# Kernel tuning notes

Hardware: AMD Instinct MI355X
Metric: run time of the kernel (lower is better)

## Reference

```python
import jax, jax.numpy as jnp
import numpy as np

N_NODES = 10000
N_EDGES = 200000
NODE_DIM = 128
EDGE_DIM = 16
CONV_DIM = 64
HEADS = 5
NEG_SLOPE = 0.2


def gatv2_layer(x, src, dst, edge_attr, Wl, bl, We, att, bias):
    # PyG GATv2Conv, share_weights=True, concat=False, add_self_loops=True, eval mode
    N = x.shape[0]
    H, C = att.shape
    xl = (x @ Wl + bl).reshape(N, H, C)  # [N,H,C]; x_r = x_l (share_weights)
    # self loops, edge_attr fill_value='mean' (mean of incoming edge_attr per node)
    deg = jax.ops.segment_sum(jnp.ones(dst.shape[0], x.dtype), dst, num_segments=N)
    loop_attr = jax.ops.segment_sum(edge_attr, dst, num_segments=N) / jnp.maximum(deg, 1.0)[:, None]
    loop = jnp.arange(N, dtype=src.dtype)
    src_f = jnp.concatenate([src, loop])
    dst_f = jnp.concatenate([dst, loop])
    ea = jnp.concatenate([edge_attr, loop_attr], axis=0)
    e_emb = (ea @ We).reshape(-1, H, C)  # [E+N,H,C]
    m = jax.nn.leaky_relu(xl[src_f] + xl[dst_f] + e_emb, NEG_SLOPE)
    score = jnp.einsum('ehc,hc->eh', m, att)  # [E+N,H]
    # per-destination softmax over incoming edges
    smax = jax.ops.segment_max(score, dst_f, num_segments=N)
    ex = jnp.exp(score - smax[dst_f])
    denom = jax.ops.segment_sum(ex, dst_f, num_segments=N)
    alpha = ex / denom[dst_f]
    out = jax.ops.segment_sum(alpha[:, :, None] * xl[src_f], dst_f, num_segments=N)
    return out.mean(axis=1) + bias  # concat=False -> mean over heads


def setup_inputs() -> dict:
    key = jax.random.key(0)
    ks = jax.random.split(key, 32)
    inp = {
        'x': jax.random.normal(ks[0], (N_NODES, NODE_DIM), jnp.float32),
        'edge_index': jax.random.randint(ks[1], (2, N_EDGES), 0, N_NODES, dtype=jnp.int32),
        'edge_attr': jax.random.normal(ks[2], (N_EDGES, EDGE_DIM), jnp.float32),
    }
    in_dims = [NODE_DIM, CONV_DIM, CONV_DIM]
    HC = HEADS * CONV_DIM
    k = 3
    for l in range(3):
        d = in_dims[l]
        inp[f'Wl{l}'] = jax.random.normal(ks[k], (d, HC), jnp.float32) / np.float32(np.sqrt(d)); k += 1
        inp[f'bl{l}'] = jnp.zeros((HC,), jnp.float32)
        inp[f'We{l}'] = jax.random.normal(ks[k], (EDGE_DIM, HC), jnp.float32) / np.float32(np.sqrt(EDGE_DIM)); k += 1
        inp[f'att{l}'] = jax.random.normal(ks[k], (HEADS, CONV_DIM), jnp.float32) / np.float32(np.sqrt(CONV_DIM)); k += 1
        inp[f'b{l}'] = jnp.zeros((CONV_DIM,), jnp.float32)
    return inp


def reference(x, edge_index, edge_attr,
              Wl0, bl0, We0, att0, b0,
              Wl1, bl1, We1, att1, b1,
              Wl2, bl2, We2, att2, b2):
    src, dst = edge_index[0], edge_index[1]
    h = x
    layers = [(Wl0, bl0, We0, att0, b0), (Wl1, bl1, We1, att1, b1), (Wl2, bl2, We2, att2, b2)]
    for Wl, bl, We, att, b in layers:
        h = gatv2_layer(h, src, dst, edge_attr, Wl, bl, We, att, b)
        h = jax.nn.elu(h)
    return h
```

## Files before the change

### kernel.cpp

```cpp
#include <hip/hip_runtime.h>
#include <hip/hip_bf16.h>


#define NN 10000
#define NE 200000
#define ND 128
#define ED 16
#define CD 64
#define NH 5
#define HC 320
#define EF 210000
#define EFP 210048
#define NEG 0.2f
#define PB 824
#define TOTB 4120
#define PERX 515

typedef float f2 __attribute__((ext_vector_type(2)));

__global__ void k_count(const int* __restrict__ dst, int* __restrict__ deg) {
  int e = blockIdx.x * blockDim.x + threadIdx.x;
  if (e >= NE) return;
  atomicAdd(&deg[dst[e]], 1);
}

__global__ __launch_bounds__(1024) void k_scan(const int* __restrict__ deg,
                                               int* __restrict__ rowptr) {
  __shared__ int part[1024];
  int t = threadIdx.x;
  int base = t * 10;
  int local[10];
  int s = 0;
  #pragma unroll
  for (int j = 0; j < 10; j++) {
    int i = base + j;
    local[j] = (i < NN) ? deg[i] : 0;
    s += local[j];
  }
  part[t] = s;
  __syncthreads();
  for (int off = 1; off < 1024; off <<= 1) {
    int v = (t >= off) ? part[t - off] : 0;
    __syncthreads();
    part[t] += v;
    __syncthreads();
  }
  int prefix = (t > 0) ? part[t - 1] : 0;
  #pragma unroll
  for (int j = 0; j < 10; j++) {
    int i = base + j;
    if (i < NN) rowptr[i] = prefix;
    prefix += local[j];
  }
  if (t == 1023) rowptr[NN] = prefix;
}

__global__ void k_fill(const int* __restrict__ ei, const int* __restrict__ rowptr,
                       int* __restrict__ cursor, int* __restrict__ csr_eid,
                       int* __restrict__ csr_src, int* __restrict__ csr_dst) {
  int e = blockIdx.x * blockDim.x + threadIdx.x;
  if (e >= NE) return;
  int d = ei[NE + e];
  int slot = atomicAdd(&cursor[d], 1);
  int pos = rowptr[d] + slot;
  csr_eid[pos] = e;
  csr_src[pos] = ei[e];
  csr_dst[pos] = d;
}

__global__ __launch_bounds__(256) void k_loopattr(const int* __restrict__ csr_eid,
                                                  const int* __restrict__ rowptr,
                                                  const float* __restrict__ eattr,
                                                  float* __restrict__ loop_attr) {
  int wave = threadIdx.x >> 6, lane = threadIdx.x & 63;
  int d = blockIdx.x * 4 + wave;
  if (d >= NN) return;
  int g = lane >> 4, k = lane & 15;
  int b = rowptr[d], n = rowptr[d + 1] - b;
  float s = 0.f;
  for (int i = g; i < n; i += 4)
    s += eattr[(size_t)csr_eid[b + i] * ED + k];
  s += __shfl_xor(s, 16, 64);
  s += __shfl_xor(s, 32, 64);
  if (g == 0) loop_attr[d * ED + k] = s / fmaxf((float)n, 1.0f);
}

__global__ void k_eacsr(const int* __restrict__ csr_eid, const float* __restrict__ eattr,
                        float* __restrict__ ea_csr) {
  int idx = blockIdx.x * blockDim.x + threadIdx.x;
  if (idx >= NE * 4) return;
  int p = idx >> 2, q = idx & 3;
  const float4* sp = (const float4*)(eattr + (size_t)csr_eid[p] * ED);
  ((float4*)(ea_csr + (size_t)p * ED))[q] = sp[q];
}

__global__ void k_wet(const float* __restrict__ We, float* __restrict__ Wpk) {
  int i = blockIdx.x * blockDim.x + threadIdx.x;
  if (i >= ED * HC) return;
  int j  = i & 1;
  int k  = (i >> 1) & 15;
  int cp = (i >> 5) & 31;
  int h  = i >> 10;
  Wpk[i] = We[k * HC + h * CD + cp * 2 + j];
}

template <int D>
__global__ __launch_bounds__(320) void k_xl(const float* __restrict__ h,
                                            const float* __restrict__ Wl,
                                            const float* __restrict__ bl,
                                            float* __restrict__ xl) {
  constexpr int NPB = 8;
  int node0 = blockIdx.x * NPB;
  int t = threadIdx.x;
  float acc[NPB];
  #pragma unroll
  for (int i = 0; i < NPB; i++) acc[i] = 0.f;
  for (int k = 0; k < D; k += 4) {
    float w0 = Wl[(k + 0) * HC + t];
    float w1 = Wl[(k + 1) * HC + t];
    float w2 = Wl[(k + 2) * HC + t];
    float w3 = Wl[(k + 3) * HC + t];
    #pragma unroll
    for (int i = 0; i < NPB; i++) {
      float4 hv = *(const float4*)(h + (size_t)(node0 + i) * D + k);
      acc[i] += hv.x * w0 + hv.y * w1 + hv.z * w2 + hv.w * w3;
    }
  }
  float bv = bl[t];
  int hh = t >> 6, c = t & 63;
  #pragma unroll
  for (int i = 0; i < NPB; i++)
    xl[((size_t)hh * NN + node0 + i) * CD + c] = acc[i] + bv;
}

__global__ __launch_bounds__(256) void k_score(
    const int* __restrict__ csr_src, const int* __restrict__ csr_dst,
    const float* __restrict__ ea_csr, const float* __restrict__ loop_attr,
    const float* __restrict__ xl, const float* __restrict__ Wpk,
    const float* __restrict__ att, float* __restrict__ wP) {
  int bid = blockIdx.x;
  int w = (bid & 7) * PERX + (bid >> 3);
  int h = w / PB;
  int lb = w - h * PB;
  int p = lb * 256 + threadIdx.x;
  if (p >= EF) return;
  int s, d;
  const float* ea;
  if (p < NE) { s = csr_src[p]; d = csr_dst[p]; ea = ea_csr + (size_t)p * ED; }
  else        { s = d = p - NE; ea = loop_attr + (size_t)(p - NE) * ED; }
  float eas[16];
  {
    const float4* q = (const float4*)ea;
    float4 t0 = q[0], t1 = q[1], t2 = q[2], t3 = q[3];
    eas[0] = t0.x;  eas[1] = t0.y;  eas[2] = t0.z;  eas[3] = t0.w;
    eas[4] = t1.x;  eas[5] = t1.y;  eas[6] = t1.z;  eas[7] = t1.w;
    eas[8] = t2.x;  eas[9] = t2.y;  eas[10] = t2.z; eas[11] = t2.w;
    eas[12] = t3.x; eas[13] = t3.y; eas[14] = t3.z; eas[15] = t3.w;
  }
  const float* xsrow = xl + ((size_t)h * NN + s) * CD;
  const float* xdrow = xl + ((size_t)h * NN + d) * CD;
  const f2* wp = (const f2*)Wpk + (size_t)h * (CD / 2) * ED;
  const f2* ap = (const f2*)(att + (size_t)h * CD);
  f2 sc2 = {0.f, 0.f};
  const f2 zero = {0.f, 0.f};
  #pragma unroll 4
  for (int cb = 0; cb < CD; cb += 4) {
    int cp = cb >> 1;
    float4 xs4 = *(const float4*)(xsrow + cb);
    float4 xd4 = *(const float4*)(xdrow + cb);
    const f2* w0 = wp + (size_t)cp * ED;
    const f2* w1 = w0 + ED;
    f2 z0 = f2{xs4.x, xs4.y} + f2{xd4.x, xd4.y};
    f2 z1 = f2{xs4.z, xs4.w} + f2{xd4.z, xd4.w};
    #pragma unroll
    for (int k = 0; k < ED; k++) {
      z0 += w0[k] * eas[k];
      z1 += w1[k] * eas[k];
    }
    z0 = __builtin_elementwise_max(z0, zero) + NEG * __builtin_elementwise_min(z0, zero);
    z1 = __builtin_elementwise_max(z1, zero) + NEG * __builtin_elementwise_min(z1, zero);
    sc2 += z0 * ap[cp];
    sc2 += z1 * ap[cp + 1];
  }
  float sc = sc2.x + sc2.y;
  sc = fminf(fmaxf(sc, -60.f), 60.f);
  wP[(size_t)h * EFP + p] = __expf(sc);
}

__global__ __launch_bounds__(320) void k_agg(
    const int* __restrict__ csr_src, const int* __restrict__ rowptr,
    const float* __restrict__ wP, const float* __restrict__ xl,
    const float* __restrict__ bias, float* __restrict__ out) {
  __shared__ float s_v[NH][CD];
  int h = threadIdx.x >> 6, lane = threadIdx.x & 63;
  int d = blockIdx.x;
  int b = rowptr[d], n = rowptr[d + 1] - b;
  const float* sp = wP + (size_t)h * EFP;
  const float* xlh = xl + (size_t)h * NN * CD + lane;
  float dn = sp[NE + d];
  float acc = dn * xlh[(size_t)d * CD];
  int p = b, pe = b + n;
  for (; p + 4 <= pe; p += 4) {
    int s0 = csr_src[p], s1 = csr_src[p + 1], s2 = csr_src[p + 2], s3 = csr_src[p + 3];
    float w0 = sp[p], w1 = sp[p + 1], w2 = sp[p + 2], w3 = sp[p + 3];
    float x0 = xlh[(size_t)s0 * CD];
    float x1 = xlh[(size_t)s1 * CD];
    float x2 = xlh[(size_t)s2 * CD];
    float x3 = xlh[(size_t)s3 * CD];
    dn += (w0 + w1) + (w2 + w3);
    acc += w0 * x0 + w1 * x1 + w2 * x2 + w3 * x3;
  }
  for (; p < pe; p++) {
    int s0 = csr_src[p];
    float w0 = sp[p];
    dn += w0;
    acc += w0 * xlh[(size_t)s0 * CD];
  }
  s_v[h][lane] = acc / dn;
  __syncthreads();
  if (h == 0) {
    float v = s_v[0][lane] + s_v[1][lane] + s_v[2][lane] + s_v[3][lane] + s_v[4][lane];
    v = v * (1.0f / NH) + bias[lane];
    v = v > 0.f ? v : expm1f(v);
    out[(size_t)d * CD + lane] = v;
  }
}

extern "C" void kernel_launch(void* const* d_in, const int* in_sizes, int n_in,
                              void* d_out, int out_size, void* d_ws, size_t ws_size,
                              hipStream_t stream) {
  const float* x = (const float*)d_in[0];
  const int* ei = (const int*)d_in[1];
  const float* eattr = (const float*)d_in[2];

  char* w = (char*)d_ws;
  int* degi      = (int*)w;                 w += NN * 4;
  int* cursor    = (int*)w;                 w += NN * 4;
  int* rowptr    = (int*)w;                 w += (NN + 1) * 4;
  int* csr_eid   = (int*)w;                 w += NE * 4;
  int* csr_src   = (int*)w;                 w += NE * 4;
  int* csr_dst   = (int*)w;                 w += NE * 4;
  float* loop_attr = (float*)w;             w += (size_t)NN * ED * 4;
  float* ea_csr  = (float*)w;               w += (size_t)NE * ED * 4;
  float* xl      = (float*)w;               w += (size_t)NN * HC * 4;
  float* wPbuf   = (float*)w;               w += (size_t)NH * EFP * 4;
  float* Wpk     = (float*)w;               w += (size_t)ED * HC * 4;
  float* hbuf    = (float*)w;               w += (size_t)NN * CD * 4;

  hipMemsetAsync(degi, 0, NN * 4, stream);
  hipMemsetAsync(cursor, 0, NN * 4, stream);
  k_count<<<(NE + 255) / 256, 256, 0, stream>>>(ei + NE, degi);
  k_scan<<<1, 1024, 0, stream>>>(degi, rowptr);
  k_fill<<<(NE + 255) / 256, 256, 0, stream>>>(ei, rowptr, cursor, csr_eid, csr_src, csr_dst);
  k_loopattr<<<(NN + 3) / 4, 256, 0, stream>>>(csr_eid, rowptr, eattr, loop_attr);
  k_eacsr<<<(NE * 4 + 255) / 256, 256, 0, stream>>>(csr_eid, eattr, ea_csr);

  for (int l = 0; l < 3; l++) {
    const float* Wl  = (const float*)d_in[3 + 5 * l];
    const float* bl  = (const float*)d_in[4 + 5 * l];
    const float* We  = (const float*)d_in[5 + 5 * l];
    const float* att = (const float*)d_in[6 + 5 * l];
    const float* b   = (const float*)d_in[7 + 5 * l];

    k_wet<<<(ED * HC + 255) / 256, 256, 0, stream>>>(We, Wpk);
    if (l == 0) k_xl<ND><<<NN / 8, 320, 0, stream>>>(x, Wl, bl, xl);
    else        k_xl<CD><<<NN / 8, 320, 0, stream>>>(hbuf, Wl, bl, xl);

    k_score<<<TOTB, 256, 0, stream>>>(csr_src, csr_dst, ea_csr, loop_attr,
                                      xl, Wpk, att, wPbuf);

    float* dst_out = (l < 2) ? hbuf : (float*)d_out;
    k_agg<<<NN, 320, 0, stream>>>(csr_src, rowptr, wPbuf, xl, b, dst_out);
  }
}
```

Before: 520.3 us.

## Restructure edge scoring to map channels to lanes with LDS reduction

The score kernel now assigns one channel per lane and 32 edges per wave instead of one edge per thread looping over all 64 channels. Each lane keeps its We column in registers, so the packed-weight kernel is removed. Edge attributes are interleaved in pairs and self-loop entries are folded into extended src/dst/ea arrays. Per-edge dot products are reduced through LDS, which makes xl row gathers coalesced across lanes. In exchange it adds a transpose through LDS, a shuffle, and extra preprocessing kernels.

```diff
diff --git a/kernel.cpp b/kernel.cpp
--- a/kernel.cpp
+++ b/kernel.cpp
@@ -12,9 +12,9 @@
 #define EF 210000
 #define EFP 210048
 #define NEG 0.2f
-#define PB 824
-#define TOTB 4120
-#define PERX 515
+#define WPH 1641
+#define TOT2 8205
+#define G2 8208
 
 typedef float f2 __attribute__((ext_vector_type(2)));
 
@@ -57,15 +57,24 @@
 
 __global__ void k_fill(const int* __restrict__ ei, const int* __restrict__ rowptr,
                        int* __restrict__ cursor, int* __restrict__ csr_eid,
-                       int* __restrict__ csr_src, int* __restrict__ csr_dst) {
+                       int* __restrict__ srcx, int* __restrict__ dstx) {
   int e = blockIdx.x * blockDim.x + threadIdx.x;
   if (e >= NE) return;
   int d = ei[NE + e];
   int slot = atomicAdd(&cursor[d], 1);
   int pos = rowptr[d] + slot;
   csr_eid[pos] = e;
-  csr_src[pos] = ei[e];
-  csr_dst[pos] = d;
+  srcx[pos] = ei[e];
+  dstx[pos] = d;
+}
+
+__global__ void k_selfext(int* __restrict__ srcx, int* __restrict__ dstx) {
+  int i = blockIdx.x * blockDim.x + threadIdx.x;
+  int p = NE + i;
+  if (p >= EFP) return;
+  int v = (p < EF) ? (p - NE) : 0;
+  srcx[p] = v;
+  dstx[p] = v;
 }
 
 __global__ __launch_bounds__(256) void k_loopattr(const int* __restrict__ csr_eid,
@@ -85,23 +94,16 @@
   if (g == 0) loop_attr[d * ED + k] = s / fmaxf((float)n, 1.0f);
 }
 
-__global__ void k_eacsr(const int* __restrict__ csr_eid, const float* __restrict__ eattr,
-                        float* __restrict__ ea_csr) {
+__global__ void k_ea2(const int* __restrict__ csr_eid, const float* __restrict__ eattr,
+                      const float* __restrict__ loop_attr, float* __restrict__ ea2) {
   int idx = blockIdx.x * blockDim.x + threadIdx.x;
-  if (idx >= NE * 4) return;
-  int p = idx >> 2, q = idx & 3;
-  const float4* sp = (const float4*)(eattr + (size_t)csr_eid[p] * ED);
-  ((float4*)(ea_csr + (size_t)p * ED))[q] = sp[q];
-}
-
-__global__ void k_wet(const float* __restrict__ We, float* __restrict__ Wpk) {
-  int i = blockIdx.x * blockDim.x + threadIdx.x;
-  if (i >= ED * HC) return;
-  int j  = i & 1;
-  int k  = (i >> 1) & 15;
-  int cp = (i >> 5) & 31;
-  int h  = i >> 10;
-  Wpk[i] = We[k * HC + h * CD + cp * 2 + j];
+  if (idx >= EFP * ED) return;
+  int p = idx >> 4, k = idx & 15;
+  float v;
+  if (p < NE)      v = eattr[(size_t)csr_eid[p] * ED + k];
+  else if (p < EF) v = loop_attr[(size_t)(p - NE) * ED + k];
+  else             v = 0.f;
+  ea2[((size_t)(p >> 1) * 32) + 2 * k + (p & 1)] = v;
 }
 
 template <int D>
@@ -134,57 +136,63 @@
 }
 
 __global__ __launch_bounds__(256) void k_score(
-    const int* __restrict__ csr_src, const int* __restrict__ csr_dst,
-    const float* __restrict__ ea_csr, const float* __restrict__ loop_attr,
-    const float* __restrict__ xl, const float* __restrict__ Wpk,
-    const float* __restrict__ att, float* __restrict__ wP) {
-  int bid = blockIdx.x;
-  int w = (bid & 7) * PERX + (bid >> 3);
-  int h = w / PB;
-  int lb = w - h * PB;
-  int p = lb * 256 + threadIdx.x;
-  if (p >= EF) return;
-  int s, d;
-  const float* ea;
-  if (p < NE) { s = csr_src[p]; d = csr_dst[p]; ea = ea_csr + (size_t)p * ED; }
-  else        { s = d = p - NE; ea = loop_attr + (size_t)(p - NE) * ED; }
-  float eas[16];
-  {
-    const float4* q = (const float4*)ea;
-    float4 t0 = q[0], t1 = q[1], t2 = q[2], t3 = q[3];
-    eas[0] = t0.x;  eas[1] = t0.y;  eas[2] = t0.z;  eas[3] = t0.w;
-    eas[4] = t1.x;  eas[5] = t1.y;  eas[6] = t1.z;  eas[7] = t1.w;
-    eas[8] = t2.x;  eas[9] = t2.y;  eas[10] = t2.z; eas[11] = t2.w;
-    eas[12] = t3.x; eas[13] = t3.y; eas[14] = t3.z; eas[15] = t3.w;
-  }
-  const float* xsrow = xl + ((size_t)h * NN + s) * CD;
-  const float* xdrow = xl + ((size_t)h * NN + d) * CD;
-  const f2* wp = (const f2*)Wpk + (size_t)h * (CD / 2) * ED;
-  const f2* ap = (const f2*)(att + (size_t)h * CD);
-  f2 sc2 = {0.f, 0.f};
+    const int* __restrict__ srcx, const int* __restrict__ dstx,
+    const float* __restrict__ ea2, const float* __restrict__ xl,
+    const float* __restrict__ We, const float* __restrict__ att,
+    float* __restrict__ wP) {
+  __shared__ float lds[4][64][34];
+  int wk = (blockIdx.x & 7) * 1026 + (blockIdx.x >> 3);
+  if (wk >= TOT2) return;
+  int h  = wk / WPH;
+  int lb = wk - h * WPH;
+  int wave = __builtin_amdgcn_readfirstlane(threadIdx.x >> 6);
+  int lane = threadIdx.x & 63;
+  int p0 = lb * 128 + wave * 32;
+
+  f2 wv[16];
+  #pragma unroll
+  for (int k = 0; k < 16; k++) {
+    float w = We[k * HC + h * CD + lane];
+    wv[k] = f2{w, w};
+  }
+  float a1 = att[h * CD + lane];
+  f2 av = f2{a1, a1};
+  const float* xh = xl + (size_t)h * NN * CD;
   const f2 zero = {0.f, 0.f};
-  #pragma unroll 4
-  for (int cb = 0; cb < CD; cb += 4) {
-    int cp = cb >> 1;
-    float4 xs4 = *(const float4*)(xsrow + cb);
-    float4 xd4 = *(const float4*)(xdrow + cb);
-    const f2* w0 = wp + (size_t)cp * ED;
-    const f2* w1 = w0 + ED;
-    f2 z0 = f2{xs4.x, xs4.y} + f2{xd4.x, xd4.y};
-    f2 z1 = f2{xs4.z, xs4.w} + f2{xd4.z, xd4.w};
+
+  f2 acc[16];
+  #pragma unroll
+  for (int i = 0; i < 16; i++) {
+    int p = p0 + 2 * i;
+    int s0 = srcx[p], s1 = srcx[p + 1];
+    int d0 = dstx[p], d1 = dstx[p + 1];
+    const f2* e = (const f2*)(ea2 + (size_t)(p >> 1) * 32);
+    float xs0 = xh[(size_t)s0 * CD + lane];
+    float xs1 = xh[(size_t)s1 * CD + lane];
+    float xd0 = xh[(size_t)d0 * CD + lane];
+    float xd1 = xh[(size_t)d1 * CD + lane];
+    f2 z = f2{xs0 + xd0, xs1 + xd1};
     #pragma unroll
-    for (int k = 0; k < ED; k++) {
-      z0 += w0[k] * eas[k];
-      z1 += w1[k] * eas[k];
-    }
-    z0 = __builtin_elementwise_max(z0, zero) + NEG * __builtin_elementwise_min(z0, zero);
-    z1 = __builtin_elementwise_max(z1, zero) + NEG * __builtin_elementwise_min(z1, zero);
-    sc2 += z0 * ap[cp];
-    sc2 += z1 * ap[cp + 1];
-  }
-  float sc = sc2.x + sc2.y;
-  sc = fminf(fmaxf(sc, -60.f), 60.f);
-  wP[(size_t)h * EFP + p] = __expf(sc);
+    for (int k = 0; k < 16; k++)
+      z += e[k] * wv[k];
+    z = __builtin_elementwise_max(z, zero) + NEG * __builtin_elementwise_min(z, zero);
+    acc[i] = z * av;
+  }
+
+  float (*L)[34] = lds[wave];
+  #pragma unroll
+  for (int i = 0; i < 16; i++)
+    *(f2*)&L[lane][2 * i] = acc[i];
+  int part = lane >> 5, j = lane & 31;
+  float sum = 0.f;
+  #pragma unroll
+  for (int r = 0; r < 32; r++)
+    sum += L[part * 32 + r][j];
+  sum += __shfl_xor(sum, 32, 64);
+  if (part == 0) {
+    float sc = fminf(fmaxf(sum, -60.f), 60.f);
+    wP[(size_t)h * EFP + p0 + j] = __expf(sc);
+  }
 }
 
 __global__ __launch_bounds__(320) void k_agg(
@@ -226,6 +234,8 @@
   }
 }
 
+static inline size_t aln(size_t x) { return (x + 255) & ~(size_t)255; }
+
 extern "C" void kernel_launch(void* const* d_in, const int* in_sizes, int n_in,
                               void* d_out, int out_size, void* d_ws, size_t ws_size,
                               hipStream_t stream) {
@@ -234,26 +244,26 @@
   const float* eattr = (const float*)d_in[2];
 
   char* w = (char*)d_ws;
-  int* degi      = (int*)w;                 w += NN * 4;
-  int* cursor    = (int*)w;                 w += NN * 4;
-  int* rowptr    = (int*)w;                 w += (NN + 1) * 4;
-  int* csr_eid   = (int*)w;                 w += NE * 4;
-  int* csr_src   = (int*)w;                 w += NE * 4;
-  int* csr_dst   = (int*)w;                 w += NE * 4;
-  float* loop_attr = (float*)w;             w += (size_t)NN * ED * 4;
-  float* ea_csr  = (float*)w;               w += (size_t)NE * ED * 4;
-  float* xl      = (float*)w;               w += (size_t)NN * HC * 4;
-  float* wPbuf   = (float*)w;               w += (size_t)NH * EFP * 4;
-  float* Wpk     = (float*)w;               w += (size_t)ED * HC * 4;
-  float* hbuf    = (float*)w;               w += (size_t)NN * CD * 4;
+  int* degi      = (int*)w;                 w += aln(NN * 4);
+  int* cursor    = (int*)w;                 w += aln(NN * 4);
+  int* rowptr    = (int*)w;                 w += aln((NN + 1) * 4);
+  int* csr_eid   = (int*)w;                 w += aln((size_t)NE * 4);
+  int* srcx      = (int*)w;                 w += aln((size_t)EFP * 4);
+  int* dstx      = (int*)w;                 w += aln((size_t)EFP * 4);
+  float* loop_attr = (float*)w;             w += aln((size_t)NN * ED * 4);
+  float* ea2     = (float*)w;               w += aln((size_t)EFP * ED * 4);
+  float* xl      = (float*)w;               w += aln((size_t)NN * HC * 4);
+  float* wPbuf   = (float*)w;               w += aln((size_t)NH * EFP * 4);
+  float* hbuf    = (float*)w;               w += aln((size_t)NN * CD * 4);
 
   hipMemsetAsync(degi, 0, NN * 4, stream);
   hipMemsetAsync(cursor, 0, NN * 4, stream);
   k_count<<<(NE + 255) / 256, 256, 0, stream>>>(ei + NE, degi);
   k_scan<<<1, 1024, 0, stream>>>(degi, rowptr);
-  k_fill<<<(NE + 255) / 256, 256, 0, stream>>>(ei, rowptr, cursor, csr_eid, csr_src, csr_dst);
+  k_fill<<<(NE + 255) / 256, 256, 0, stream>>>(ei, rowptr, cursor, csr_eid, srcx, dstx);
+  k_selfext<<<(EFP - NE + 255) / 256, 256, 0, stream>>>(srcx, dstx);
   k_loopattr<<<(NN + 3) / 4, 256, 0, stream>>>(csr_eid, rowptr, eattr, loop_attr);
-  k_eacsr<<<(NE * 4 + 255) / 256, 256, 0, stream>>>(csr_eid, eattr, ea_csr);
+  k_ea2<<<(EFP * ED + 255) / 256, 256, 0, stream>>>(csr_eid, eattr, loop_attr, ea2);
 
   for (int l = 0; l < 3; l++) {
     const float* Wl  = (const float*)d_in[3 + 5 * l];
@@ -262,14 +272,12 @@
     const float* att = (const float*)d_in[6 + 5 * l];
     const float* b   = (const float*)d_in[7 + 5 * l];
 
-    k_wet<<<(ED * HC + 255) / 256, 256, 0, stream>>>(We, Wpk);
     if (l == 0) k_xl<ND><<<NN / 8, 320, 0, stream>>>(x, Wl, bl, xl);
     else        k_xl<CD><<<NN / 8, 320, 0, stream>>>(hbuf, Wl, bl, xl);
 
-    k_score<<<TOTB, 256, 0, stream>>>(csr_src, csr_dst, ea_csr, loop_attr,
-                                      xl, Wpk, att, wPbuf);
+    k_score<<<G2, 256, 0, stream>>>(srcx, dstx, ea2, xl, We, att, wPbuf);
 
     float* dst_out = (l < 2) ? hbuf : (float*)d_out;
-    k_agg<<<NN, 320, 0, stream>>>(csr_src, rowptr, wPbuf, xl, b, dst_out);
-  }
-}
+    k_agg<<<NN, 320, 0, stream>>>(srcx, rowptr, wPbuf, xl, b, dst_out);
+  }
+}
```

Result: slower. 532.5 us (+2.4%).

## Split aggregation into per-head wave work with atomic accumulation and combine kernel

Applied to the files above, without the earlier changes.

The per-destination aggregation kernel, which used a 320-thread block for five heads plus a shared-memory reduction, is replaced. Each 64-lane wave now handles one (head, node) pair and atomically adds its normalized contribution into a zeroed buffer. Block indices are remapped so that the same head's work is spread across the eight XCDs. A separate elementwise kernel then applies the head mean, bias and ELU. This adds a memset, float atomics and an extra launch per layer in exchange for finer-grained scheduling, and writes the combine output in place over hbuf when l<2.

```diff
diff --git a/kernel.cpp b/kernel.cpp
--- a/kernel.cpp
+++ b/kernel.cpp
@@ -15,6 +15,9 @@
 #define PB 824
 #define TOTB 4120
 #define PERX 515
+#define NW_AGG 50000
+#define BL_AGG 12504
+#define PERXA 1563
 
 typedef float f2 __attribute__((ext_vector_type(2)));
 
@@ -187,13 +190,17 @@
   wP[(size_t)h * EFP + p] = __expf(sc);
 }
 
-__global__ __launch_bounds__(320) void k_agg(
+__global__ __launch_bounds__(256) void k_agg2(
     const int* __restrict__ csr_src, const int* __restrict__ rowptr,
     const float* __restrict__ wP, const float* __restrict__ xl,
-    const float* __restrict__ bias, float* __restrict__ out) {
-  __shared__ float s_v[NH][CD];
-  int h = threadIdx.x >> 6, lane = threadIdx.x & 63;
-  int d = blockIdx.x;
+    float* __restrict__ accum) {
+  int bid = blockIdx.x;
+  int b2 = (bid & 7) * PERXA + (bid >> 3);
+  int wv = threadIdx.x >> 6, lane = threadIdx.x & 63;
+  int g = b2 * 4 + wv;
+  if (g >= NW_AGG) return;
+  int h = g / NN;
+  int d = g - h * NN;
   int b = rowptr[d], n = rowptr[d + 1] - b;
   const float* sp = wP + (size_t)h * EFP;
   const float* xlh = xl + (size_t)h * NN * CD + lane;
@@ -216,15 +223,21 @@
     dn += w0;
     acc += w0 * xlh[(size_t)s0 * CD];
   }
-  s_v[h][lane] = acc / dn;
-  __syncthreads();
-  if (h == 0) {
-    float v = s_v[0][lane] + s_v[1][lane] + s_v[2][lane] + s_v[3][lane] + s_v[4][lane];
-    v = v * (1.0f / NH) + bias[lane];
-    v = v > 0.f ? v : expm1f(v);
-    out[(size_t)d * CD + lane] = v;
-  }
-}
+  atomicAdd(&accum[(size_t)d * CD + lane], acc / dn);
+}
+
+__global__ __launch_bounds__(256) void k_comb(const float* accum,
+                                              const float* __restrict__ bias,
+                                              float* out) {
+  int idx = blockIdx.x * blockDim.x + threadIdx.x;
+  if (idx >= NN * CD) return;
+  int c = idx & (CD - 1);
+  float v = accum[idx] * (1.0f / NH) + bias[c];
+  v = v > 0.f ? v : expm1f(v);
+  out[idx] = v;
+}
+
+static inline size_t aln(size_t x) { return (x + 255) & ~(size_t)255; }
 
 extern "C" void kernel_launch(void* const* d_in, const int* in_sizes, int n_in,
                               void* d_out, int out_size, void* d_ws, size_t ws_size,
@@ -234,18 +247,18 @@
   const float* eattr = (const float*)d_in[2];
 
   char* w = (char*)d_ws;
-  int* degi      = (int*)w;                 w += NN * 4;
-  int* cursor    = (int*)w;                 w += NN * 4;
-  int* rowptr    = (int*)w;                 w += (NN + 1) * 4;
-  int* csr_eid   = (int*)w;                 w += NE * 4;
-  int* csr_src   = (int*)w;                 w += NE * 4;
-  int* csr_dst   = (int*)w;                 w += NE * 4;
-  float* loop_attr = (float*)w;             w += (size_t)NN * ED * 4;
-  float* ea_csr  = (float*)w;               w += (size_t)NE * ED * 4;
-  float* xl      = (float*)w;               w += (size_t)NN * HC * 4;
-  float* wPbuf   = (float*)w;               w += (size_t)NH * EFP * 4;
-  float* Wpk     = (float*)w;               w += (size_t)ED * HC * 4;
-  float* hbuf    = (float*)w;               w += (size_t)NN * CD * 4;
+  int* degi      = (int*)w;                 w += aln(NN * 4);
+  int* cursor    = (int*)w;                 w += aln(NN * 4);
+  int* rowptr    = (int*)w;                 w += aln((NN + 1) * 4);
+  int* csr_eid   = (int*)w;                 w += aln((size_t)NE * 4);
+  int* csr_src   = (int*)w;                 w += aln((size_t)NE * 4);
+  int* csr_dst   = (int*)w;                 w += aln((size_t)NE * 4);
+  float* loop_attr = (float*)w;             w += aln((size_t)NN * ED * 4);
+  float* ea_csr  = (float*)w;               w += aln((size_t)NE * ED * 4);
+  float* xl      = (float*)w;               w += aln((size_t)NN * HC * 4);
+  float* wPbuf   = (float*)w;               w += aln((size_t)NH * EFP * 4);
+  float* Wpk     = (float*)w;               w += aln((size_t)ED * HC * 4);
+  float* hbuf    = (float*)w;               w += aln((size_t)NN * CD * 4);
 
   hipMemsetAsync(degi, 0, NN * 4, stream);
   hipMemsetAsync(cursor, 0, NN * 4, stream);
@@ -266,10 +279,14 @@
     if (l == 0) k_xl<ND><<<NN / 8, 320, 0, stream>>>(x, Wl, bl, xl);
     else        k_xl<CD><<<NN / 8, 320, 0, stream>>>(hbuf, Wl, bl, xl);
 
+    hipMemsetAsync(hbuf, 0, (size_t)NN * CD * 4, stream);
+
     k_score<<<TOTB, 256, 0, stream>>>(csr_src, csr_dst, ea_csr, loop_attr,
                                       xl, Wpk, att, wPbuf);
 
+    k_agg2<<<BL_AGG, 256, 0, stream>>>(csr_src, rowptr, wPbuf, xl, hbuf);
+
     float* dst_out = (l < 2) ? hbuf : (float*)d_out;
-    k_agg<<<NN, 320, 0, stream>>>(csr_src, rowptr, wPbuf, xl, b, dst_out);
-  }
-}
+    k_comb<<<(NN * CD + 255) / 256, 256, 0, stream>>>(hbuf, b, dst_out);
+  }
+}
```

After: 505.9 us. 1.03x faster.

## Store xl node-major and compute loop_attr from the reordered edge attributes

Applied to the files above, without the earlier changes.

Changes the xl buffer from a head-major [H][N][C] layout to a node-major [N][H*C] layout, so each node's rows for all heads sit together and k_xl writes are contiguous per thread. k_loopattr now reads the already-gathered CSR-ordered edge attributes instead of gathering through csr_eid, and it runs after k_eacsr. Workspace buffers are aligned to 256 bytes. The layout change alters locality in k_score and k_agg, since the head-major blocks of score and aggregation now stride across a larger buffer, which may help or hurt cache reuse.

```diff
diff --git a/kernel.cpp b/kernel.cpp
--- a/kernel.cpp
+++ b/kernel.cpp
@@ -68,9 +68,17 @@
   csr_dst[pos] = d;
 }
 
-__global__ __launch_bounds__(256) void k_loopattr(const int* __restrict__ csr_eid,
+__global__ void k_eacsr(const int* __restrict__ csr_eid, const float* __restrict__ eattr,
+                        float* __restrict__ ea_csr) {
+  int idx = blockIdx.x * blockDim.x + threadIdx.x;
+  if (idx >= NE * 4) return;
+  int p = idx >> 2, q = idx & 3;
+  const float4* sp = (const float4*)(eattr + (size_t)csr_eid[p] * ED);
+  ((float4*)(ea_csr + (size_t)p * ED))[q] = sp[q];
+}
+
+__global__ __launch_bounds__(256) void k_loopattr(const float* __restrict__ ea_csr,
                                                   const int* __restrict__ rowptr,
-                                                  const float* __restrict__ eattr,
                                                   float* __restrict__ loop_attr) {
   int wave = threadIdx.x >> 6, lane = threadIdx.x & 63;
   int d = blockIdx.x * 4 + wave;
@@ -79,19 +87,10 @@
   int b = rowptr[d], n = rowptr[d + 1] - b;
   float s = 0.f;
   for (int i = g; i < n; i += 4)
-    s += eattr[(size_t)csr_eid[b + i] * ED + k];
+    s += ea_csr[(size_t)(b + i) * ED + k];
   s += __shfl_xor(s, 16, 64);
   s += __shfl_xor(s, 32, 64);
   if (g == 0) loop_attr[d * ED + k] = s / fmaxf((float)n, 1.0f);
-}
-
-__global__ void k_eacsr(const int* __restrict__ csr_eid, const float* __restrict__ eattr,
-                        float* __restrict__ ea_csr) {
-  int idx = blockIdx.x * blockDim.x + threadIdx.x;
-  if (idx >= NE * 4) return;
-  int p = idx >> 2, q = idx & 3;
-  const float4* sp = (const float4*)(eattr + (size_t)csr_eid[p] * ED);
-  ((float4*)(ea_csr + (size_t)p * ED))[q] = sp[q];
 }
 
 __global__ void k_wet(const float* __restrict__ We, float* __restrict__ Wpk) {
@@ -127,10 +126,9 @@
     }
   }
   float bv = bl[t];
-  int hh = t >> 6, c = t & 63;
   #pragma unroll
   for (int i = 0; i < NPB; i++)
-    xl[((size_t)hh * NN + node0 + i) * CD + c] = acc[i] + bv;
+    xl[(size_t)(node0 + i) * HC + t] = acc[i] + bv;
 }
 
 __global__ __launch_bounds__(256) void k_score(
@@ -157,8 +155,8 @@
     eas[8] = t2.x;  eas[9] = t2.y;  eas[10] = t2.z; eas[11] = t2.w;
     eas[12] = t3.x; eas[13] = t3.y; eas[14] = t3.z; eas[15] = t3.w;
   }
-  const float* xsrow = xl + ((size_t)h * NN + s) * CD;
-  const float* xdrow = xl + ((size_t)h * NN + d) * CD;
+  const float* xsrow = xl + (size_t)s * HC + h * CD;
+  const float* xdrow = xl + (size_t)d * HC + h * CD;
   const f2* wp = (const f2*)Wpk + (size_t)h * (CD / 2) * ED;
   const f2* ap = (const f2*)(att + (size_t)h * CD);
   f2 sc2 = {0.f, 0.f};
@@ -196,17 +194,17 @@
   int d = blockIdx.x;
   int b = rowptr[d], n = rowptr[d + 1] - b;
   const float* sp = wP + (size_t)h * EFP;
-  const float* xlh = xl + (size_t)h * NN * CD + lane;
+  const float* xlh = xl + h * CD + lane;
   float dn = sp[NE + d];
-  float acc = dn * xlh[(size_t)d * CD];
+  float acc = dn * xlh[(size_t)d * HC];
   int p = b, pe = b + n;
   for (; p + 4 <= pe; p += 4) {
     int s0 = csr_src[p], s1 = csr_src[p + 1], s2 = csr_src[p + 2], s3 = csr_src[p + 3];
     float w0 = sp[p], w1 = sp[p + 1], w2 = sp[p + 2], w3 = sp[p + 3];
-    float x0 = xlh[(size_t)s0 * CD];
-    float x1 = xlh[(size_t)s1 * CD];
-    float x2 = xlh[(size_t)s2 * CD];
-    float x3 = xlh[(size_t)s3 * CD];
+    float x0 = xlh[(size_t)s0 * HC];
+    float x1 = xlh[(size_t)s1 * HC];
+    float x2 = xlh[(size_t)s2 * HC];
+    float x3 = xlh[(size_t)s3 * HC];
     dn += (w0 + w1) + (w2 + w3);
     acc += w0 * x0 + w1 * x1 + w2 * x2 + w3 * x3;
   }
@@ -214,7 +212,7 @@
     int s0 = csr_src[p];
     float w0 = sp[p];
     dn += w0;
-    acc += w0 * xlh[(size_t)s0 * CD];
+    acc += w0 * xlh[(size_t)s0 * HC];
   }
   s_v[h][lane] = acc / dn;
   __syncthreads();
@@ -226,6 +224,8 @@
   }
 }
 
+static inline size_t aln(size_t x) { return (x + 255) & ~(size_t)255; }
+
 extern "C" void kernel_launch(void* const* d_in, const int* in_sizes, int n_in,
                               void* d_out, int out_size, void* d_ws, size_t ws_size,
                               hipStream_t stream) {
@@ -234,26 +234,26 @@
   const float* eattr = (const float*)d_in[2];
 
   char* w = (char*)d_ws;
-  int* degi      = (int*)w;                 w += NN * 4;
-  int* cursor    = (int*)w;                 w += NN * 4;
-  int* rowptr    = (int*)w;                 w += (NN + 1) * 4;
-  int* csr_eid   = (int*)w;                 w += NE * 4;
-  int* csr_src   = (int*)w;                 w += NE * 4;
-  int* csr_dst   = (int*)w;                 w += NE * 4;
-  float* loop_attr = (float*)w;             w += (size_t)NN * ED * 4;
-  float* ea_csr  = (float*)w;               w += (size_t)NE * ED * 4;
-  float* xl      = (float*)w;               w += (size_t)NN * HC * 4;
-  float* wPbuf   = (float*)w;               w += (size_t)NH * EFP * 4;
-  float* Wpk     = (float*)w;               w += (size_t)ED * HC * 4;
-  float* hbuf    = (float*)w;               w += (size_t)NN * CD * 4;
+  int* degi      = (int*)w;                 w += aln(NN * 4);
+  int* cursor    = (int*)w;                 w += aln(NN * 4);
+  int* rowptr    = (int*)w;                 w += aln((NN + 1) * 4);
+  int* csr_eid   = (int*)w;                 w += aln((size_t)NE * 4);
+  int* csr_src   = (int*)w;                 w += aln((size_t)NE * 4);
+  int* csr_dst   = (int*)w;                 w += aln((size_t)NE * 4);
+  float* loop_attr = (float*)w;             w += aln((size_t)NN * ED * 4);
+  float* ea_csr  = (float*)w;               w += aln((size_t)NE * ED * 4);
+  float* xl      = (float*)w;               w += aln((size_t)NN * HC * 4);
+  float* wPbuf   = (float*)w;               w += aln((size_t)NH * EFP * 4);
+  float* Wpk     = (float*)w;               w += aln((size_t)ED * HC * 4);
+  float* hbuf    = (float*)w;               w += aln((size_t)NN * CD * 4);
 
   hipMemsetAsync(degi, 0, NN * 4, stream);
   hipMemsetAsync(cursor, 0, NN * 4, stream);
   k_count<<<(NE + 255) / 256, 256, 0, stream>>>(ei + NE, degi);
   k_scan<<<1, 1024, 0, stream>>>(degi, rowptr);
   k_fill<<<(NE + 255) / 256, 256, 0, stream>>>(ei, rowptr, cursor, csr_eid, csr_src, csr_dst);
-  k_loopattr<<<(NN + 3) / 4, 256, 0, stream>>>(csr_eid, rowptr, eattr, loop_attr);
   k_eacsr<<<(NE * 4 + 255) / 256, 256, 0, stream>>>(csr_eid, eattr, ea_csr);
+  k_loopattr<<<(NN + 3) / 4, 256, 0, stream>>>(ea_csr, rowptr, loop_attr);
 
   for (int l = 0; l < 3; l++) {
     const float* Wl  = (const float*)d_in[3 + 5 * l];
```

Result: faster. 471.3 us (-9.4%).
